# Performance work log

Hardware: AMD Instinct MI355X
Metric: run time of the kernel (lower is better)

Reference implementation:

```python
import jax, jax.numpy as jnp
import numpy as np

N_NODES = 50000
N_EDGES = 800000
N_LABEL = 200000
IN_C, HID_C, OUT_C = 128, 128, 64


def setup_inputs() -> dict:
    key = jax.random.key(0)
    ks = jax.random.split(key, 9)
    s = lambda fan_in: 1.0 / np.sqrt(fan_in)
    return {
        "x": jax.random.normal(ks[0], (N_NODES, IN_C), jnp.float32),
        "W1": jax.random.normal(ks[1], (IN_C, HID_C), jnp.float32) * s(IN_C),
        "b1": jnp.zeros((HID_C,), jnp.float32),
        "W2": jax.random.normal(ks[2], (HID_C, HID_C), jnp.float32) * s(HID_C),
        "b2": jnp.zeros((HID_C,), jnp.float32),
        "W3": jax.random.normal(ks[3], (HID_C, OUT_C), jnp.float32) * s(HID_C),
        "b3": jnp.zeros((OUT_C,), jnp.float32),
        "edge_index": jax.random.randint(ks[4], (2, N_EDGES), 0, N_NODES, jnp.int32),
        "edge_label_index": jax.random.randint(ks[5], (2, N_LABEL), 0, N_NODES, jnp.int32),
    }


def _gcn_conv(x, W, b, src, dst, dinv, num_nodes):
    # x @ W then symmetric-normalized scatter-sum over edges (self-loops included in src/dst)
    h = x @ W                                  # [N, out]
    norm = dinv[src] * dinv[dst]               # [E+N]
    msgs = h[src] * norm[:, None]              # [E+N, out]
    out = jax.ops.segment_sum(msgs, dst, num_segments=num_nodes)
    return out + b


def _encode(x, W1, b1, W2, b2, W3, b3, edge_index, num_nodes):
    loops = jnp.arange(num_nodes, dtype=edge_index.dtype)
    src = jnp.concatenate([edge_index[0], loops])
    dst = jnp.concatenate([edge_index[1], loops])
    # degree (with self-loops) at targets; deg >= 1 so rsqrt is safe
    deg = jax.ops.segment_sum(jnp.ones(dst.shape[0], x.dtype), dst, num_segments=num_nodes)
    dinv = jax.lax.rsqrt(deg)
    z = _gcn_conv(x, W1, b1, src, dst, dinv, num_nodes)
    z = jax.nn.relu(z)  # dropout treated as eval-mode identity
    z = _gcn_conv(z, W2, b2, src, dst, dinv, num_nodes)
    z = jax.nn.relu(z)
    z = _gcn_conv(z, W3, b3, src, dst, dinv, num_nodes)
    return z


def reference(x, W1, b1, W2, b2, W3, b3, edge_index, edge_label_index):
    z = _encode(x, W1, b1, W2, b2, W3, b3, edge_index, N_NODES)
    # decode: gather both endpoints, elementwise mul, sum over feature dim
    return (z[edge_label_index[0]] * z[edge_label_index[1]]).sum(axis=-1)
```

## Files before the change

### kernel.cpp

```cpp
#include <hip/hip_runtime.h>

#define N_NODES 50000
#define N_EDGES 800000
#define N_LABEL 200000
#define ROW_BLOCKS 782

typedef __attribute__((ext_vector_type(4))) float f32x4;
typedef _Float16 f16;
typedef __attribute__((ext_vector_type(8))) _Float16 f16x8;


__global__ __launch_bounds__(256)
void k_zero(int4* __restrict__ p, int n4) {
    int i = blockIdx.x * 256 + threadIdx.x;
    if (i < n4) p[i] = int4{0, 0, 0, 0};
}

__global__ __launch_bounds__(256)
void k_prep(const float* __restrict__ W1, const float* __restrict__ W2,
            const float* __restrict__ W3,
            f16* WT1h, f16* WT1l, f16* WT2h, f16* WT2l, f16* WT3h, f16* WT3l,
            const int* __restrict__ dst, int* cnt) {
    int b = blockIdx.x, tid = threadIdx.x;
    if (b < 64) {
        int t = b * 256 + tid;
        int c = t >> 7, k = t & 127;
        float w = W1[k * 128 + c];
        f16 h = (f16)w;
        WT1h[c * 128 + k] = h; WT1l[c * 128 + k] = (f16)(w - (float)h);
        w = W2[k * 128 + c];
        h = (f16)w;
        WT2h[c * 128 + k] = h; WT2l[c * 128 + k] = (f16)(w - (float)h);
        if (c < 64) {
            w = W3[k * 64 + c];
            h = (f16)w;
            WT3h[c * 128 + k] = h; WT3l[c * 128 + k] = (f16)(w - (float)h);
        }
    } else {
        int vb = b - 64;
        int g = vb & 7;
        int i = (vb >> 3) * 256 + tid;
        int d = dst[i];
        if ((unsigned)(d - g * 6250) < 6250u) atomicAdd(&cnt[d], 1);
    }
}

__global__ __launch_bounds__(256)
void k_partial(const int* __restrict__ cnt, float* __restrict__ dinv,
               int* __restrict__ bsum, int N) {
    __shared__ int wsum[4];
    int b = blockIdx.x, t = threadIdx.x;
    int i = b * 256 + t;
    int v = (i < N) ? cnt[i] : 0;
    if (i < N) dinv[i] = rsqrtf((float)v + 1.0f);
    int s = v;
#pragma unroll
    for (int d = 1; d < 64; d <<= 1) s += __shfl_xor(s, d, 64);
    if ((t & 63) == 0) wsum[t >> 6] = s;
    __syncthreads();
    if (t == 0) bsum[b] = wsum[0] + wsum[1] + wsum[2] + wsum[3];
}

__global__ __launch_bounds__(256)
void k_offsets(const int* __restrict__ cnt, const int* __restrict__ bsum,
               int* __restrict__ off, int N, int NB) {
    __shared__ int wsum[4];
    __shared__ int add0_s;
    int b = blockIdx.x, t = threadIdx.x;
    int v0 = (t < b && t < NB) ? bsum[t] : 0;
    int s0 = v0;
#pragma unroll
    for (int d = 1; d < 64; d <<= 1) s0 += __shfl_xor(s0, d, 64);
    if ((t & 63) == 0) wsum[t >> 6] = s0;
    __syncthreads();
    if (t == 0) add0_s = wsum[0] + wsum[1] + wsum[2] + wsum[3];
    __syncthreads();
    int add = add0_s;
    __syncthreads();
    int i = b * 256 + t;
    int v = (i < N) ? cnt[i] : 0;
    int lane = t & 63, w = t >> 6;
    int sv = v;
#pragma unroll
    for (int d = 1; d < 64; d <<= 1) {
        int u = __shfl_up(sv, d, 64);
        if (lane >= d) sv += u;
    }
    if (lane == 63) wsum[w] = sv;
    __syncthreads();
    for (int ww = 0; ww < w; ++ww) add += wsum[ww];
    if (i < N) off[i + 1] = add + sv;
    if (i == 0) off[0] = 0;
}

__global__ __launch_bounds__(256)
void k_bucket(const int* __restrict__ srcv, const int* __restrict__ dstv,
              const int* __restrict__ off, int* cnt2, unsigned short* __restrict__ csr) {
    int vb = blockIdx.x;
    int g = vb & 7;
    int i = (vb >> 3) * 256 + threadIdx.x;
    int d = dstv[i];
    if ((unsigned)(d - g * 6250) < 6250u) {
        int slot = off[d] + atomicAdd(&cnt2[d], 1);
        csr[slot] = (unsigned short)srcv[i];
    }
}

__global__ __launch_bounds__(256)
void k_gemm1(const float* __restrict__ x,
             const f16* __restrict__ WTh, const f16* __restrict__ WTl,
             const float* __restrict__ dinv, f16* __restrict__ As, int N) {
    constexpr int NCB = 4;
    __shared__ f16 Hs[64 * 136];
    __shared__ f16 Ls[64 * 136];
    int b = blockIdx.x;
    int c0 = (b & 1) * 64;
    int t = threadIdx.x;

#pragma unroll
    for (int i = 0; i < 4; ++i) {
        int ch = t + i * 256;
        int col = ch >> 4;
        int kc = (ch & 15) * 8;
        *(f16x8*)&Hs[col * 136 + kc] = *(const f16x8*)&WTh[(long)(c0 + col) * 128 + kc];
        *(f16x8*)&Ls[col * 136 + kc] = *(const f16x8*)&WTl[(long)(c0 + col) * 128 + kc];
    }

    int wv = t >> 6, l = t & 63;
    int r0w = (b >> 1) * 64 + wv * 16;
    int arow = r0w + (l & 15);
    if (arow >= N) arow = N - 1;
    int kb = (l >> 4) * 8;

    f16x8 ah[4], al[4];
#pragma unroll
    for (int ks = 0; ks < 4; ++ks) {
        const float* xp = &x[(long)arow * 128 + ks * 32 + kb];
        float4 a0 = *(const float4*)xp;
        float4 a1 = *(const float4*)(xp + 4);
        float fv[8] = {a0.x, a0.y, a0.z, a0.w, a1.x, a1.y, a1.z, a1.w};
#pragma unroll
        for (int j = 0; j < 8; ++j) {
            f16 h = (f16)fv[j];
            ah[ks][j] = h;
            al[ks][j] = (f16)(fv[j] - (float)h);
        }
    }
    __syncthreads();

    f32x4 acc[NCB];
#pragma unroll
    for (int cb = 0; cb < NCB; ++cb) acc[cb] = f32x4{0.f, 0.f, 0.f, 0.f};
#pragma unroll
    for (int ks = 0; ks < 4; ++ks) {
#pragma unroll
        for (int cb = 0; cb < NCB; ++cb) {
            int wi = (cb * 16 + (l & 15)) * 136 + ks * 32 + kb;
            f16x8 bh = *(const f16x8*)&Hs[wi];
            f16x8 bl = *(const f16x8*)&Ls[wi];
            acc[cb] = __builtin_amdgcn_mfma_f32_16x16x32_f16(ah[ks], bh, acc[cb], 0, 0, 0);
            acc[cb] = __builtin_amdgcn_mfma_f32_16x16x32_f16(ah[ks], bl, acc[cb], 0, 0, 0);
            acc[cb] = __builtin_amdgcn_mfma_f32_16x16x32_f16(al[ks], bh, acc[cb], 0, 0, 0);
        }
    }
    int rbase = r0w + (l >> 4) * 4;
    float dv[4];
#pragma unroll
    for (int i = 0; i < 4; ++i) dv[i] = (rbase + i < N) ? dinv[rbase + i] : 0.f;
#pragma unroll
    for (int cb = 0; cb < NCB; ++cb) {
        int fc = c0 + cb * 16 + (l & 15);
        long sb = (long)(fc >> 5) * N_NODES * 32 + (fc & 31);
#pragma unroll
        for (int i = 0; i < 4; ++i) {
            int r = rbase + i;
            if (r < N) As[sb + (long)r * 32] = (f16)(acc[cb][i] * dv[i]);
        }
    }
}

template<int M>
__global__ __launch_bounds__(256)
void k_gemm23(const f16* __restrict__ Bs,
              const f16* __restrict__ WTh, const f16* __restrict__ WTl,
              const float* __restrict__ dinv, f16* __restrict__ As, int N) {
    constexpr int NCB = M / 32;
    constexpr int HC = M / 2;
    __shared__ f16 Hs[HC * 136];
    __shared__ f16 Ls[HC * 136];
    int b = blockIdx.x;
    int c0 = (b & 1) * HC;
    int t = threadIdx.x;

#pragma unroll
    for (int i = 0; i < HC / 16; ++i) {
        int ch = t + i * 256;
        int col = ch >> 4;
        int kc = (ch & 15) * 8;
        *(f16x8*)&Hs[col * 136 + kc] = *(const f16x8*)&WTh[(long)(c0 + col) * 128 + kc];
        *(f16x8*)&Ls[col * 136 + kc] = *(const f16x8*)&WTl[(long)(c0 + col) * 128 + kc];
    }

    int wv = t >> 6, l = t & 63;
    int r0w = (b >> 1) * 64 + wv * 16;
    int arow = r0w + (l & 15);
    if (arow >= N) arow = N - 1;
    int kb = (l >> 4) * 8;

    f16x8 a[4];
#pragma unroll
    for (int ks = 0; ks < 4; ++ks)
        a[ks] = *(const f16x8*)&Bs[((long)ks * N_NODES + arow) * 32 + kb];
    __syncthreads();

    f32x4 acc[NCB];
#pragma unroll
    for (int cb = 0; cb < NCB; ++cb) acc[cb] = f32x4{0.f, 0.f, 0.f, 0.f};
#pragma unroll
    for (int ks = 0; ks < 4; ++ks) {
#pragma unroll
        for (int cb = 0; cb < NCB; ++cb) {
            int wi = (cb * 16 + (l & 15)) * 136 + ks * 32 + kb;
            f16x8 bh = *(const f16x8*)&Hs[wi];
            f16x8 bl = *(const f16x8*)&Ls[wi];
            acc[cb] = __builtin_amdgcn_mfma_f32_16x16x32_f16(a[ks], bh, acc[cb], 0, 0, 0);
            acc[cb] = __builtin_amdgcn_mfma_f32_16x16x32_f16(a[ks], bl, acc[cb], 0, 0, 0);
        }
    }
    int rbase = r0w + (l >> 4) * 4;
    float dv[4];
#pragma unroll
    for (int i = 0; i < 4; ++i) dv[i] = (rbase + i < N) ? dinv[rbase + i] : 0.f;
#pragma unroll
    for (int cb = 0; cb < NCB; ++cb) {
        int fc = c0 + cb * 16 + (l & 15);
        long sb = (long)(fc >> 5) * N_NODES * 32 + (fc & 31);
#pragma unroll
        for (int i = 0; i < 4; ++i) {
            int r = rbase + i;
            if (r < N) As[sb + (long)r * 32] = (f16)(acc[cb][i] * dv[i]);
        }
    }
}

__global__ __launch_bounds__(256)
void k_gather128(const f16* __restrict__ As, const int* __restrict__ off,
                 const unsigned short* __restrict__ csr, const float* __restrict__ dinv,
                 const float* __restrict__ bias, f16* __restrict__ Bs) {
    int vb = blockIdx.x;
    int g = vb & 7, blk = vb >> 3;
    int t = threadIdx.x;
    int nl = blk * 64 + (t >> 2);
    if (nl >= 25000) return;
    int node = (g & 1) * 25000 + nl;
    int cs = g >> 1;
    int qq = (t & 3) * 8;
    const f16* Aq = As + (long)cs * N_NODES * 32 + qq;

    float acc[8];
    {
        f16x8 v = *(const f16x8*)&Aq[(long)node * 32];
#pragma unroll
        for (int c = 0; c < 8; ++c) acc[c] = (float)v[c];
    }
    int j = off[node], j1 = off[node + 1];
    for (; j + 8 <= j1; j += 8) {
        int s0 = csr[j + 0], s1 = csr[j + 1], s2 = csr[j + 2], s3 = csr[j + 3];
        int s4 = csr[j + 4], s5 = csr[j + 5], s6 = csr[j + 6], s7 = csr[j + 7];
        f16x8 v0 = *(const f16x8*)&Aq[(long)s0 * 32];
        f16x8 v1 = *(const f16x8*)&Aq[(long)s1 * 32];
        f16x8 v2 = *(const f16x8*)&Aq[(long)s2 * 32];
        f16x8 v3 = *(const f16x8*)&Aq[(long)s3 * 32];
        f16x8 v4 = *(const f16x8*)&Aq[(long)s4 * 32];
        f16x8 v5 = *(const f16x8*)&Aq[(long)s5 * 32];
        f16x8 v6 = *(const f16x8*)&Aq[(long)s6 * 32];
        f16x8 v7 = *(const f16x8*)&Aq[(long)s7 * 32];
#pragma unroll
        for (int c = 0; c < 8; ++c)
            acc[c] += ((float)v0[c] + (float)v1[c] + (float)v2[c] + (float)v3[c])
                    + ((float)v4[c] + (float)v5[c] + (float)v6[c] + (float)v7[c]);
    }
    for (; j + 2 <= j1; j += 2) {
        int s0 = csr[j + 0], s1 = csr[j + 1];
        f16x8 v0 = *(const f16x8*)&Aq[(long)s0 * 32];
        f16x8 v1 = *(const f16x8*)&Aq[(long)s1 * 32];
#pragma unroll
        for (int c = 0; c < 8; ++c) acc[c] += (float)v0[c] + (float)v1[c];
    }
    if (j < j1) {
        int s = csr[j];
        f16x8 v = *(const f16x8*)&Aq[(long)s * 32];
#pragma unroll
        for (int c = 0; c < 8; ++c) acc[c] += (float)v[c];
    }
    float sc = dinv[node];
    int q = cs * 32 + qq;
    float4 bb0 = *(const float4*)&bias[q];
    float4 bb1 = *(const float4*)&bias[q + 4];
    float bv[8] = {bb0.x, bb0.y, bb0.z, bb0.w, bb1.x, bb1.y, bb1.z, bb1.w};
    f16x8 o;
#pragma unroll
    for (int c = 0; c < 8; ++c) o[c] = (f16)fmaxf(acc[c] * sc + bv[c], 0.f);
    *(f16x8*)&Bs[((long)cs * N_NODES + node) * 32 + qq] = o;
}

__global__ __launch_bounds__(256)
void k_gather64(const f16* __restrict__ As, const int* __restrict__ off,
                const unsigned short* __restrict__ csr, const float* __restrict__ dinv,
                const float* __restrict__ bias, f16* __restrict__ z) {
    int vb = blockIdx.x;
    int g = vb & 7, blk = vb >> 3;
    int t = threadIdx.x;
    int nl = blk * 64 + (t >> 2);
    if (nl >= 12500) return;
    int node = (g >> 1) * 12500 + nl;
    int cs = g & 1;
    int qq = (t & 3) * 8;
    const f16* Aq = As + (long)cs * N_NODES * 32 + qq;

    float acc[8];
    {
        f16x8 v = *(const f16x8*)&Aq[(long)node * 32];
#pragma unroll
        for (int c = 0; c < 8; ++c) acc[c] = (float)v[c];
    }
    int j = off[node], j1 = off[node + 1];
    for (; j + 8 <= j1; j += 8) {
        int s0 = csr[j + 0], s1 = csr[j + 1], s2 = csr[j + 2], s3 = csr[j + 3];
        int s4 = csr[j + 4], s5 = csr[j + 5], s6 = csr[j + 6], s7 = csr[j + 7];
        f16x8 v0 = *(const f16x8*)&Aq[(long)s0 * 32];
        f16x8 v1 = *(const f16x8*)&Aq[(long)s1 * 32];
        f16x8 v2 = *(const f16x8*)&Aq[(long)s2 * 32];
        f16x8 v3 = *(const f16x8*)&Aq[(long)s3 * 32];
        f16x8 v4 = *(const f16x8*)&Aq[(long)s4 * 32];
        f16x8 v5 = *(const f16x8*)&Aq[(long)s5 * 32];
        f16x8 v6 = *(const f16x8*)&Aq[(long)s6 * 32];
        f16x8 v7 = *(const f16x8*)&Aq[(long)s7 * 32];
#pragma unroll
        for (int c = 0; c < 8; ++c)
            acc[c] += ((float)v0[c] + (float)v1[c] + (float)v2[c] + (float)v3[c])
                    + ((float)v4[c] + (float)v5[c] + (float)v6[c] + (float)v7[c]);
    }
    for (; j + 2 <= j1; j += 2) {
        int s0 = csr[j + 0], s1 = csr[j + 1];
        f16x8 v0 = *(const f16x8*)&Aq[(long)s0 * 32];
        f16x8 v1 = *(const f16x8*)&Aq[(long)s1 * 32];
#pragma unroll
        for (int c = 0; c < 8; ++c) acc[c] += (float)v0[c] + (float)v1[c];
    }
    if (j < j1) {
        int s = csr[j];
        f16x8 v = *(const f16x8*)&Aq[(long)s * 32];
#pragma unroll
        for (int c = 0; c < 8; ++c) acc[c] += (float)v[c];
    }
    float sc = dinv[node];
    int q = cs * 32 + qq;
    float4 bb0 = *(const float4*)&bias[q];
    float4 bb1 = *(const float4*)&bias[q + 4];
    float bv[8] = {bb0.x, bb0.y, bb0.z, bb0.w, bb1.x, bb1.y, bb1.z, bb1.w};
    f16x8 o;
#pragma unroll
    for (int c = 0; c < 8; ++c) o[c] = (f16)(acc[c] * sc + bv[c]);
    *(f16x8*)&z[(long)node * 64 + q] = o;
}

__global__ __launch_bounds__(256)
void k_decode(const f16* __restrict__ z, const int* __restrict__ eli,
              float* __restrict__ out, int L) {
    int t = blockIdx.x * blockDim.x + threadIdx.x;
    int e = t >> 3;
    int lane = t & 7;
    if (e >= L) return;
    int a = eli[e], b = eli[L + e];
    f16x8 va = *(const f16x8*)&z[(long)a * 64 + lane * 8];
    f16x8 vb = *(const f16x8*)&z[(long)b * 64 + lane * 8];
    float s = 0.f;
#pragma unroll
    for (int c = 0; c < 8; ++c) s += (float)va[c] * (float)vb[c];
    s += __shfl_xor(s, 1, 8);
    s += __shfl_xor(s, 2, 8);
    s += __shfl_xor(s, 4, 8);
    if (lane == 0) out[e] = s;
}

extern "C" void kernel_launch(void* const* d_in, const int* in_sizes, int n_in,
                              void* d_out, int out_size, void* d_ws, size_t ws_size,
                              hipStream_t stream) {
    const float* x   = (const float*)d_in[0];
    const float* W1  = (const float*)d_in[1];
    const float* b1  = (const float*)d_in[2];
    const float* W2  = (const float*)d_in[3];
    const float* b2  = (const float*)d_in[4];
    const float* W3  = (const float*)d_in[5];
    const float* b3  = (const float*)d_in[6];
    const int*   ei  = (const int*)d_in[7];
    const int*   eli = (const int*)d_in[8];
    float* out = (float*)d_out;

    char* ws = (char*)d_ws;
    float* dinv = (float*)ws;                  ws += 50048 * 4;
    f16*   A    = (f16*)ws;                    ws += (long)N_NODES * 128 * 2;
    f16*   B    = (f16*)ws;                    ws += (long)N_NODES * 128 * 2;
    f16*   z    = (f16*)ws;                    ws += (long)N_NODES * 64 * 2;
    int*   cnt  = (int*)ws;                    ws += 50048 * 4;
    int*   cnt2 = (int*)ws;                    ws += 50048 * 4;
    int*   off  = (int*)ws;                    ws += 50048 * 4;
    unsigned short* csr = (unsigned short*)ws; ws += (long)N_EDGES * 2;
    int*   bsum = (int*)ws;                    ws += 256 * 4;
    f16*   WT1h = (f16*)ws;                    ws += 16384 * 2;
    f16*   WT1l = (f16*)ws;                    ws += 16384 * 2;
    f16*   WT2h = (f16*)ws;                    ws += 16384 * 2;
    f16*   WT2l = (f16*)ws;                    ws += 16384 * 2;
    f16*   WT3h = (f16*)ws;                    ws += 8192 * 2;
    f16*   WT3l = (f16*)ws;                    ws += 8192 * 2;

    const int* esrc = ei;
    const int* edst = ei + N_EDGES;

    const int NB = (N_NODES + 255) / 256;

    k_zero   <<<98, 256, 0, stream>>>((int4*)cnt, 25024);
    k_prep   <<<25064, 256, 0, stream>>>(W1, W2, W3, WT1h, WT1l, WT2h, WT2l,
                                         WT3h, WT3l, edst, cnt);
    k_partial<<<NB, 256, 0, stream>>>(cnt, dinv, bsum, N_NODES);
    k_offsets<<<NB, 256, 0, stream>>>(cnt, bsum, off, N_NODES, NB);
    k_bucket <<<25000, 256, 0, stream>>>(esrc, edst, off, cnt2, csr);

    k_gemm1<<<ROW_BLOCKS * 2, 256, 0, stream>>>(x, WT1h, WT1l, dinv, A, N_NODES);
    k_gather128<<<391 * 8, 256, 0, stream>>>(A, off, csr, dinv, b1, B);
    k_gemm23<128><<<ROW_BLOCKS * 2, 256, 0, stream>>>(B, WT2h, WT2l, dinv, A, N_NODES);
    k_gather128<<<391 * 8, 256, 0, stream>>>(A, off, csr, dinv, b2, B);
    k_gemm23<64><<<ROW_BLOCKS * 2, 256, 0, stream>>>(B, WT3h, WT3l, dinv, A, N_NODES);
    k_gather64<<<196 * 8, 256, 0, stream>>>(A, off, csr, dinv, b3, z);

    k_decode<<<(N_LABEL * 8 + 255) / 256, 256, 0, stream>>>(z, eli, out, N_LABEL);
}
```

Before: 205.1 us.

## Use XCD-aware persistent work-stealing in gather kernels for L2 locality

The gather kernels become persistent: a fixed grid of blocks reads its hardware XCC id and pulls chunks from a per-group atomic counter. Each block starts on the feature slice (group) matching its XCD and moves to other groups only once that one is drained. The aim is to keep each slice of the feature table resident in one XCD's L2 and to balance uneven degree work. In exchange it adds an atomic and two barriers per chunk, and it relies on the counters being zeroed, which the enlarged zero kernel now covers.

```diff
diff --git a/kernel.cpp b/kernel.cpp
--- a/kernel.cpp
+++ b/kernel.cpp
@@ -4,11 +4,18 @@
 #define N_EDGES 800000
 #define N_LABEL 200000
 #define ROW_BLOCKS 782
+#define GATHER_GRID 1536
 
 typedef __attribute__((ext_vector_type(4))) float f32x4;
 typedef _Float16 f16;
 typedef __attribute__((ext_vector_type(8))) _Float16 f16x8;
 
+
+__device__ __forceinline__ int xcc_id() {
+    int x;
+    asm volatile("s_getreg_b32 %0, hwreg(HW_REG_XCC_ID, 0, 4)" : "=s"(x));
+    return x & 7;
+}
 
 __global__ __launch_bounds__(256)
 void k_zero(int4* __restrict__ p, int n4) {
@@ -243,13 +250,11 @@
     }
 }
 
-__global__ __launch_bounds__(256)
-void k_gather128(const f16* __restrict__ As, const int* __restrict__ off,
-                 const unsigned short* __restrict__ csr, const float* __restrict__ dinv,
-                 const float* __restrict__ bias, f16* __restrict__ Bs) {
-    int vb = blockIdx.x;
-    int g = vb & 7, blk = vb >> 3;
-    int t = threadIdx.x;
+__device__ __forceinline__
+void gather128_body(const f16* __restrict__ As, const int* __restrict__ off,
+                    const unsigned short* __restrict__ csr, const float* __restrict__ dinv,
+                    const float* __restrict__ bias, f16* __restrict__ Bs,
+                    int g, int blk, int t) {
     int nl = blk * 64 + (t >> 2);
     if (nl >= 25000) return;
     int node = (g & 1) * 25000 + nl;
@@ -305,12 +310,31 @@
 }
 
 __global__ __launch_bounds__(256)
-void k_gather64(const f16* __restrict__ As, const int* __restrict__ off,
-                const unsigned short* __restrict__ csr, const float* __restrict__ dinv,
-                const float* __restrict__ bias, f16* __restrict__ z) {
-    int vb = blockIdx.x;
-    int g = vb & 7, blk = vb >> 3;
+void k_gather128(const f16* __restrict__ As, const int* __restrict__ off,
+                 const unsigned short* __restrict__ csr, const float* __restrict__ dinv,
+                 const float* __restrict__ bias, f16* __restrict__ Bs,
+                 int* __restrict__ ctr8) {
+    __shared__ int chunk_s;
+    int xcd = xcc_id();
     int t = threadIdx.x;
+    for (int pass = 0; pass < 8; ++pass) {
+        int g = (xcd + pass) & 7;
+        while (true) {
+            __syncthreads();
+            if (t == 0) chunk_s = atomicAdd(&ctr8[g], 1);
+            __syncthreads();
+            int chunk = chunk_s;
+            if (chunk >= 391) break;
+            gather128_body(As, off, csr, dinv, bias, Bs, g, chunk, t);
+        }
+    }
+}
+
+__device__ __forceinline__
+void gather64_body(const f16* __restrict__ As, const int* __restrict__ off,
+                   const unsigned short* __restrict__ csr, const float* __restrict__ dinv,
+                   const float* __restrict__ bias, f16* __restrict__ z,
+                   int g, int blk, int t) {
     int nl = blk * 64 + (t >> 2);
     if (nl >= 12500) return;
     int node = (g >> 1) * 12500 + nl;
@@ -363,6 +387,27 @@
 #pragma unroll
     for (int c = 0; c < 8; ++c) o[c] = (f16)(acc[c] * sc + bv[c]);
     *(f16x8*)&z[(long)node * 64 + q] = o;
+}
+
+__global__ __launch_bounds__(256)
+void k_gather64(const f16* __restrict__ As, const int* __restrict__ off,
+                const unsigned short* __restrict__ csr, const float* __restrict__ dinv,
+                const float* __restrict__ bias, f16* __restrict__ z,
+                int* __restrict__ ctr8) {
+    __shared__ int chunk_s;
+    int xcd = xcc_id();
+    int t = threadIdx.x;
+    for (int pass = 0; pass < 8; ++pass) {
+        int g = (xcd + pass) & 7;
+        while (true) {
+            __syncthreads();
+            if (t == 0) chunk_s = atomicAdd(&ctr8[g], 1);
+            __syncthreads();
+            int chunk = chunk_s;
+            if (chunk >= 196) break;
+            gather64_body(As, off, csr, dinv, bias, z, g, chunk, t);
+        }
+    }
 }
 
 __global__ __launch_bounds__(256)
@@ -405,6 +450,7 @@
     f16*   z    = (f16*)ws;                    ws += (long)N_NODES * 64 * 2;
     int*   cnt  = (int*)ws;                    ws += 50048 * 4;
     int*   cnt2 = (int*)ws;                    ws += 50048 * 4;
+    int*   ctr  = (int*)ws;                    ws += 32 * 4;
     int*   off  = (int*)ws;                    ws += 50048 * 4;
     unsigned short* csr = (unsigned short*)ws; ws += (long)N_EDGES * 2;
     int*   bsum = (int*)ws;                    ws += 256 * 4;
@@ -420,7 +466,7 @@
 
     const int NB = (N_NODES + 255) / 256;
 
-    k_zero   <<<98, 256, 0, stream>>>((int4*)cnt, 25024);
+    k_zero   <<<98, 256, 0, stream>>>((int4*)cnt, 25032);
     k_prep   <<<25064, 256, 0, stream>>>(W1, W2, W3, WT1h, WT1l, WT2h, WT2l,
                                          WT3h, WT3l, edst, cnt);
     k_partial<<<NB, 256, 0, stream>>>(cnt, dinv, bsum, N_NODES);
@@ -428,11 +474,11 @@
     k_bucket <<<25000, 256, 0, stream>>>(esrc, edst, off, cnt2, csr);
 
     k_gemm1<<<ROW_BLOCKS * 2, 256, 0, stream>>>(x, WT1h, WT1l, dinv, A, N_NODES);
-    k_gather128<<<391 * 8, 256, 0, stream>>>(A, off, csr, dinv, b1, B);
+    k_gather128<<<GATHER_GRID, 256, 0, stream>>>(A, off, csr, dinv, b1, B, ctr);
     k_gemm23<128><<<ROW_BLOCKS * 2, 256, 0, stream>>>(B, WT2h, WT2l, dinv, A, N_NODES);
-    k_gather128<<<391 * 8, 256, 0, stream>>>(A, off, csr, dinv, b2, B);
+    k_gather128<<<GATHER_GRID, 256, 0, stream>>>(A, off, csr, dinv, b2, B, ctr + 8);
     k_gemm23<64><<<ROW_BLOCKS * 2, 256, 0, stream>>>(B, WT3h, WT3l, dinv, A, N_NODES);
-    k_gather64<<<196 * 8, 256, 0, stream>>>(A, off, csr, dinv, b3, z);
+    k_gather64<<<GATHER_GRID, 256, 0, stream>>>(A, off, csr, dinv, b3, z, ctr + 16);
 
     k_decode<<<(N_LABEL * 8 + 255) / 256, 256, 0, stream>>>(z, eli, out, N_LABEL);
 }
```

New measurement: 670.8 us. 227% more time.
